# Kernel optimization log

Hardware: AMD Instinct MI355X
Metric: run time of the kernel (lower is better)

The kernel has to match this reference:

```python
import jax, jax.numpy as jnp
import numpy as np

B, S, D = 16, 2048, 768  # batch, padded subword length, roberta hidden dim


def setup_inputs() -> dict:
    key = jax.random.key(0)
    k1, k2 = jax.random.split(key)
    robert_embed = jax.random.normal(k1, (B, S, D), dtype=jnp.float32)
    # Non-decreasing per-row segment ids: contiguous runs of equal ids are the
    # subword spans that merge_list would average; singleton runs pass through.
    seg_ids = jnp.sort(jax.random.randint(k2, (B, S), 0, S, dtype=jnp.int32), axis=-1)
    return {"robert_embed": robert_embed, "seg_ids": seg_ids}


def reference(robert_embed, seg_ids):
    # Segment-mean gather/scatter: out[b, w] = mean_{p: seg_ids[b,p]==w} x[b, p]
    b, s, d = robert_embed.shape
    w = s  # output word slots (<= s); empty slots yield zeros
    flat_seg = (seg_ids + (w * jnp.arange(b, dtype=seg_ids.dtype))[:, None]).reshape(-1)
    x_flat = robert_embed.reshape(-1, d)
    sums = jax.ops.segment_sum(x_flat, flat_seg, num_segments=b * w)  # [b*w, d]
    counts = jax.ops.segment_sum(
        jnp.ones((b * s,), dtype=robert_embed.dtype), flat_seg, num_segments=b * w
    )
    out = sums / jnp.maximum(counts, 1)[:, None]
    return out.reshape(b, w, d)
```

## Files before the change

### kernel.cpp

```cpp
#include <hip/hip_runtime.h>

#define BB 16
#define SS 2048
#define DD 768
#define D4 (DD / 4)
#define CH 8

#define ADD4(A, R) { A.x += R.x; A.y += R.y; A.z += R.z; A.w += R.w; }

typedef __attribute__((ext_vector_type(4))) float f32x4;

__device__ __forceinline__ void nt_store(float4 v, float4* p) {
    f32x4 t; t.x = v.x; t.y = v.y; t.z = v.z; t.w = v.w;
    __builtin_nontemporal_store(t, (f32x4*)p);
}

__device__ __forceinline__ void emit_row(float* __restrict__ ob, int v, int vnext,
                                         int c, float4 a0, float4 a1, float4 a2,
                                         int lane) {
    float inv = 1.0f / (float)c;
    a0.x *= inv; a0.y *= inv; a0.z *= inv; a0.w *= inv;
    a1.x *= inv; a1.y *= inv; a1.z *= inv; a1.w *= inv;
    a2.x *= inv; a2.y *= inv; a2.z *= inv; a2.w *= inv;
    float4* op = (float4*)(ob + (size_t)v * DD);
    nt_store(a0, op + lane);
    nt_store(a1, op + lane + 64);
    nt_store(a2, op + lane + 128);
    const float4 zz = make_float4(0.f, 0.f, 0.f, 0.f);
    for (int z = v + 1; z < vnext; ++z) {
        float4* zp = (float4*)(ob + (size_t)z * DD);
        nt_store(zz, zp + lane);
        nt_store(zz, zp + lane + 64);
        nt_store(zz, zp + lane + 128);
    }
}

__global__ __launch_bounds__(256, 4) void seg_mean_v4(
    const float* __restrict__ x,
    const int*   __restrict__ seg,
    float*       __restrict__ out) {
    int lane = threadIdx.x & 63;
    int wave = threadIdx.x >> 6;
    int gw   = (blockIdx.x << 2) + wave;
    int p0   = gw * CH;
    int b    = p0 >> 11;
    int q0   = p0 & (SS - 1);
    const int*   srow = seg + (b << 11);
    const float* xb   = x   + (size_t)(b << 11) * DD;
    float*       ob   = out + (size_t)(b << 11) * DD;

    float4 r[CH][3];
    #pragma unroll
    for (int j = 0; j < CH; ++j) {
        const float4* xp = (const float4*)(xb + (size_t)(q0 + j) * DD);
        r[j][0] = xp[lane];
        r[j][1] = xp[lane + 64];
        r[j][2] = xp[lane + 128];
    }

    int  myv = 0;
    bool startl = false;
    if (lane < CH) {
        int p = q0 + lane;
        myv = srow[p];
        int pv = (p == 0) ? (myv ^ 1) : srow[p - 1];
        startl = (myv != pv);
    }
    unsigned long long smask = __ballot(startl);

    if (q0 == 0) {
        int first = srow[0];
        const float4 zz = make_float4(0.f, 0.f, 0.f, 0.f);
        for (int z = 0; z < first; ++z) {
            float4* zp = (float4*)(ob + (size_t)z * DD);
            nt_store(zz, zp + lane);
            nt_store(zz, zp + lane + 64);
            nt_store(zz, zp + lane + 128);
        }
    }
    if (!smask) return;

    int i0 = (int)__builtin_ctzll(smask);

    float4 a0 = make_float4(0.f,0.f,0.f,0.f), a1 = a0, a2 = a0;
    int s_rel = 0, vcur = 0;
    #pragma unroll
    for (int j = 0; j < CH; ++j) {
        if (j >= i0) {
            if ((smask >> j) & 1) {
                s_rel = j;
                vcur  = __shfl(myv, j);
                a0 = r[j][0]; a1 = r[j][1]; a2 = r[j][2];
            } else {
                ADD4(a0, r[j][0]); ADD4(a1, r[j][1]); ADD4(a2, r[j][2]);
            }
            if (j + 1 < CH && ((smask >> (j + 1)) & 1)) {
                int vnext = __shfl(myv, j + 1);
                emit_row(ob, vcur, vnext, j + 1 - s_rel, a0, a1, a2, lane);
            }
        }
    }

    int ilast = 63 - (int)__builtin_clzll(smask);
    int e = q0 + CH;
    if (e < SS) {
        for (;;) {
            int idx = e + lane;
            int vv  = (idx < SS) ? srow[idx] : (vcur ^ 1);
            unsigned long long m  = __ballot(vv == vcur);
            unsigned long long nm = ~m;
            if (nm) { e += (int)__builtin_ctzll(nm); break; }
            e += 64;
        }
    }
    for (int t = q0 + CH; t < e; ++t) {
        const float4* xn = (const float4*)(xb + (size_t)t * DD);
        float4 t0 = xn[lane], t1 = xn[lane + 64], t2 = xn[lane + 128];
        ADD4(a0, t0); ADD4(a1, t1); ADD4(a2, t2);
    }
    int vnext = (e < SS) ? srow[e] : SS;
    emit_row(ob, vcur, vnext, e - (q0 + ilast), a0, a1, a2, lane);
}

extern "C" void kernel_launch(void* const* d_in, const int* in_sizes, int n_in,
                              void* d_out, int out_size, void* d_ws, size_t ws_size,
                              hipStream_t stream) {
    const float* x   = (const float*)d_in[0];
    const int*   seg = (const int*)d_in[1];
    float* out = (float*)d_out;

    int nBlocks = (BB * SS) / (4 * CH);
    seg_mean_v4<<<nBlocks, 256, 0, stream>>>(x, seg, out);
}
```

Before: 180.3 us.

## Stage 16-row block tiles in LDS via direct global-to-LDS loads

Each block now loads 16 consecutive rows of x straight into shared memory with global_load_lds, split across its four waves, then synchronises once. Each wave handles the segment starts that fall in its quarter of the tile and reduces each segment from LDS, so a segment that spans wave boundaries no longer needs register chaining. The goal is to issue loads asynchronously without going through VGPRs and to spread segment work across waves. In exchange it uses 48KB of LDS per block, which limits occupancy, adds a block barrier, and segments that run past the tile still read the rest from global memory.

```diff
diff --git a/kernel.cpp b/kernel.cpp
--- a/kernel.cpp
+++ b/kernel.cpp
@@ -4,7 +4,8 @@
 #define SS 2048
 #define DD 768
 #define D4 (DD / 4)
-#define CH 8
+#define RB 16
+#define RW 4
 
 #define ADD4(A, R) { A.x += R.x; A.y += R.y; A.z += R.z; A.w += R.w; }
 
@@ -14,6 +15,11 @@
     f32x4 t; t.x = v.x; t.y = v.y; t.z = v.z; t.w = v.w;
     __builtin_nontemporal_store(t, (f32x4*)p);
 }
+
+#define GLOAD_LDS16(gaddr, laddr)                                              \
+    __builtin_amdgcn_global_load_lds(                                          \
+        (const __attribute__((address_space(1))) void*)(gaddr),                \
+        (__attribute__((address_space(3))) void*)(laddr), 16, 0, 0)
 
 __device__ __forceinline__ void emit_row(float* __restrict__ ob, int v, int vnext,
                                          int c, float4 a0, float4 a1, float4 a2,
@@ -35,32 +41,32 @@
     }
 }
 
-__global__ __launch_bounds__(256, 4) void seg_mean_v4(
+__global__ __launch_bounds__(256) void seg_mean_v5(
     const float* __restrict__ x,
     const int*   __restrict__ seg,
     float*       __restrict__ out) {
+    __shared__ float lds[RB * DD];
     int lane = threadIdx.x & 63;
-    int wave = threadIdx.x >> 6;
-    int gw   = (blockIdx.x << 2) + wave;
-    int p0   = gw * CH;
+    int wv   = threadIdx.x >> 6;
+    int p0   = blockIdx.x * RB;
     int b    = p0 >> 11;
     int q0   = p0 & (SS - 1);
     const int*   srow = seg + (b << 11);
     const float* xb   = x   + (size_t)(b << 11) * DD;
     float*       ob   = out + (size_t)(b << 11) * DD;
 
-    float4 r[CH][3];
-    #pragma unroll
-    for (int j = 0; j < CH; ++j) {
-        const float4* xp = (const float4*)(xb + (size_t)(q0 + j) * DD);
-        r[j][0] = xp[lane];
-        r[j][1] = xp[lane + 64];
-        r[j][2] = xp[lane + 128];
+    {
+        const float* gsrc = xb + (size_t)(q0 + wv * RW) * DD + lane * 4;
+        float*       ldst = lds + (wv * RW) * DD;
+        #pragma unroll
+        for (int k = 0; k < RW * 3; ++k) {
+            GLOAD_LDS16(gsrc + k * 256, ldst + k * 256);
+        }
     }
 
     int  myv = 0;
     bool startl = false;
-    if (lane < CH) {
+    if (lane < RB) {
         int p = q0 + lane;
         myv = srow[p];
         int pv = (p == 0) ? (myv ^ 1) : srow[p - 1];
@@ -68,7 +74,7 @@
     }
     unsigned long long smask = __ballot(startl);
 
-    if (q0 == 0) {
+    if (q0 == 0 && wv == 0) {
         int first = srow[0];
         const float4 zz = make_float4(0.f, 0.f, 0.f, 0.f);
         for (int z = 0; z < first; ++z) {
@@ -78,48 +84,55 @@
             nt_store(zz, zp + lane + 128);
         }
     }
-    if (!smask) return;
 
-    int i0 = (int)__builtin_ctzll(smask);
+    __syncthreads();
 
-    float4 a0 = make_float4(0.f,0.f,0.f,0.f), a1 = a0, a2 = a0;
-    int s_rel = 0, vcur = 0;
-    #pragma unroll
-    for (int j = 0; j < CH; ++j) {
-        if (j >= i0) {
-            if ((smask >> j) & 1) {
-                s_rel = j;
-                vcur  = __shfl(myv, j);
-                a0 = r[j][0]; a1 = r[j][1]; a2 = r[j][2];
-            } else {
-                ADD4(a0, r[j][0]); ADD4(a1, r[j][1]); ADD4(a2, r[j][2]);
+    unsigned wmask = (unsigned)(smask >> (wv * RW)) & ((1u << RW) - 1);
+    while (wmask) {
+        int jrel = __builtin_ctz(wmask); wmask &= wmask - 1;
+        int j    = wv * RW + jrel;
+        int vcur = __shfl(myv, j);
+
+        unsigned long long above = smask >> (j + 1);
+        int  e_loc;
+        bool tail;
+        if (above) { e_loc = j + 1 + (int)__builtin_ctzll(above); tail = false; }
+        else       { e_loc = RB;                                  tail = true;  }
+
+        const float4* lp = (const float4*)(lds + (size_t)j * DD);
+        float4 a0 = lp[lane], a1 = lp[lane + 64], a2 = lp[lane + 128];
+        for (int t = j + 1; t < e_loc; ++t) {
+            const float4* q = (const float4*)(lds + (size_t)t * DD);
+            float4 r0 = q[lane], r1 = q[lane + 64], r2 = q[lane + 128];
+            ADD4(a0, r0); ADD4(a1, r1); ADD4(a2, r2);
+        }
+
+        int c, vnext;
+        if (!tail) {
+            c     = e_loc - j;
+            vnext = __shfl(myv, e_loc);
+        } else {
+            int e = q0 + RB;
+            if (e < SS) {
+                for (;;) {
+                    int idx = e + lane;
+                    int vv  = (idx < SS) ? srow[idx] : (vcur ^ 1);
+                    unsigned long long m  = __ballot(vv == vcur);
+                    unsigned long long nm = ~m;
+                    if (nm) { e += (int)__builtin_ctzll(nm); break; }
+                    e += 64;
+                }
             }
-            if (j + 1 < CH && ((smask >> (j + 1)) & 1)) {
-                int vnext = __shfl(myv, j + 1);
-                emit_row(ob, vcur, vnext, j + 1 - s_rel, a0, a1, a2, lane);
+            for (int t = q0 + RB; t < e; ++t) {
+                const float4* xn = (const float4*)(xb + (size_t)t * DD);
+                float4 r0 = xn[lane], r1 = xn[lane + 64], r2 = xn[lane + 128];
+                ADD4(a0, r0); ADD4(a1, r1); ADD4(a2, r2);
             }
+            c     = e - (q0 + j);
+            vnext = (e < SS) ? srow[e] : SS;
         }
+        emit_row(ob, vcur, vnext, c, a0, a1, a2, lane);
     }
-
-    int ilast = 63 - (int)__builtin_clzll(smask);
-    int e = q0 + CH;
-    if (e < SS) {
-        for (;;) {
-            int idx = e + lane;
-            int vv  = (idx < SS) ? srow[idx] : (vcur ^ 1);
-            unsigned long long m  = __ballot(vv == vcur);
-            unsigned long long nm = ~m;
-            if (nm) { e += (int)__builtin_ctzll(nm); break; }
-            e += 64;
-        }
-    }
-    for (int t = q0 + CH; t < e; ++t) {
-        const float4* xn = (const float4*)(xb + (size_t)t * DD);
-        float4 t0 = xn[lane], t1 = xn[lane + 64], t2 = xn[lane + 128];
-        ADD4(a0, t0); ADD4(a1, t1); ADD4(a2, t2);
-    }
-    int vnext = (e < SS) ? srow[e] : SS;
-    emit_row(ob, vcur, vnext, e - (q0 + ilast), a0, a1, a2, lane);
 }
 
 extern "C" void kernel_launch(void* const* d_in, const int* in_sizes, int n_in,
@@ -129,6 +142,6 @@
     const int*   seg = (const int*)d_in[1];
     float* out = (float*)d_out;
 
-    int nBlocks = (BB * SS) / (4 * CH);
-    seg_mean_v4<<<nBlocks, 256, 0, stream>>>(x, seg, out);
+    int nBlocks = (BB * SS) / RB;
+    seg_mean_v5<<<nBlocks, 256, 0, stream>>>(x, seg, out);
 }
```

New measurement: 179.3 us. About the same (-0.6%).
